# Optimization experiments

Measured on AMD Instinct MI355X. Metric: run time of the kernel, lower is better.

Reference implementation:

```python
import jax, jax.numpy as jnp
import numpy as np

B, G, N_IN, N_HID, N_OUT = 2, 4096, 8, 32, 32
ALPHA, BETA, BN_EPS = 0.005, 5e-5, 1e-5
EDGE_P = 0.05  # adjacency density


def _lin_init(k, fan_in, fan_out):
    k1, k2 = jax.random.split(k)
    lim = 1.0 / np.sqrt(fan_in)
    W = jax.random.uniform(k1, (fan_in, fan_out), minval=-lim, maxval=lim, dtype=jnp.float32)
    b = jax.random.uniform(k2, (fan_out,), minval=-lim, maxval=lim, dtype=jnp.float32)
    return W, b


def setup_inputs() -> dict:
    key = jax.random.key(0)
    ks = jax.random.split(key, 12)
    W_infer, b_infer = _lin_init(ks[0], N_IN, N_HID)
    W_e1, b_e1 = _lin_init(ks[1], 2 * N_HID, 1)
    W_e2, b_e2 = _lin_init(ks[2], 2 * N_HID, 1)
    W_n1, b_n1 = _lin_init(ks[3], 2 * N_HID, N_OUT)
    W_n2, b_n2 = _lin_init(ks[4], 2 * N_HID, N_OUT)
    W_m1, b_m1 = _lin_init(ks[5], 2 * N_HID, N_OUT)
    W_m2, b_m2 = _lin_init(ks[6], 2 * N_HID, N_OUT)
    x = jax.random.normal(ks[7], (B, G, N_IN), dtype=jnp.float32)
    edges1 = jax.random.bernoulli(ks[8], EDGE_P, (G, G)).astype(jnp.float32)
    edges2 = jax.random.bernoulli(ks[9], EDGE_P, (G, G)).astype(jnp.float32)
    bn_gamma = jnp.ones((G,), jnp.float32)
    bn_beta = jnp.zeros((G,), jnp.float32)
    return dict(x=x, edges1=edges1, edges2=edges2, W_infer=W_infer, b_infer=b_infer,
                W_e1=W_e1, b_e1=b_e1, W_e2=W_e2, b_e2=b_e2,
                W_n1=W_n1, b_n1=b_n1, W_n2=W_n2, b_n2=b_n2,
                W_m1=W_m1, b_m1=b_m1, W_m2=W_m2, b_m2=b_m2,
                bn_gamma=bn_gamma, bn_beta=bn_beta)


def _mp_block(x, adj, coef, W_e, b_e, W_n, b_n, W_m, b_m):
    # x: [B,G,H]. Torch builds edge feature at flat index k=i*G+j as cat([x_j, x_i])
    # (shape2 = col gather, shape1 = row gather). We keep the same math without
    # materializing the [B,G*G,2H] tensor.
    Hh = x.shape[-1]
    s_src = x @ W_e[:Hh]   # [B,G,1]  (x_j part of mlp_edge)
    s_dst = x @ W_e[Hh:]   # [B,G,1]  (x_i part of mlp_edge)
    logits = s_dst[:, :, None, 0] + s_src[:, None, :, 0] + b_e[0]   # [B,G,G] at (i,j)
    w = adj + coef * (adj == 0).astype(x.dtype)                     # ori_edge + coef*thres_edge
    e = jax.nn.sigmoid(logits) * w[None]                            # [B,G,G]
    # receive at node i: sum_j e_ij * [x_j, x_i]
    recv_src = jnp.einsum('bij,bjh->bih', e, x)                     # sum_j e_ij x_j
    recv_dst = x * jnp.sum(e, axis=2)[..., None]                    # x_i * sum_j e_ij
    recv = jnp.concatenate([recv_src, recv_dst], axis=-1)           # [B,G,2H]
    recv = jax.nn.elu(recv @ W_n + b_n)                             # nodes_mlp + elu
    upd = jnp.concatenate([recv, x], axis=-1) @ W_m + b_m           # mesg_merge (mode='cat')
    return jax.nn.elu(upd)


def _forward(x, edges1, edges2, W_infer, b_infer, W_e1, b_e1, W_e2, b_e2,
             W_n1, b_n1, W_n2, b_n2, W_m1, b_m1, W_m2, b_m2, bn_gamma, bn_beta):
    h = jax.nn.elu(x @ W_infer + b_infer)                           # infer + elu, [B,G,H]
    h = _mp_block(h, edges1, ALPHA, W_e1, b_e1, W_n1, b_n1, W_m1, b_m1)
    # BatchNorm1d(gene_num) on [B, G, n_out]: per-gene stats over (batch, feature)
    mu = jnp.mean(h, axis=(0, 2), keepdims=True)
    var = jnp.var(h, axis=(0, 2), keepdims=True)
    h = (h - mu) * jax.lax.rsqrt(var + BN_EPS)
    h = h * bn_gamma[None, :, None] + bn_beta[None, :, None]
    return _mp_block(h, edges2, BETA, W_e2, b_e2, W_n2, b_n2, W_m2, b_m2)


def reference(x, edges1, edges2, W_infer, b_infer, W_e1, b_e1, W_e2, b_e2,
              W_n1, b_n1, W_n2, b_n2, W_m1, b_m1, W_m2, b_m2, bn_gamma, bn_beta):
    return _forward(x, edges1, edges2, W_infer, b_infer, W_e1, b_e1, W_e2, b_e2,
                    W_n1, b_n1, W_n2, b_n2, W_m1, b_m1, W_m2, b_m2, bn_gamma, bn_beta)
```

## Files before the change

kernel.cpp:

```cpp
#include <hip/hip_runtime.h>

#define G 4096
#define BSZ 2
#define NIN 8
#define HID 32
#define NLOG2E (-1.4426950408889634f)

typedef __attribute__((ext_vector_type(8))) short short8;
typedef __attribute__((ext_vector_type(4))) float floatx4;
typedef unsigned short ushort_t;
typedef unsigned int uint_t;

__device__ __forceinline__ float elu1(float v) {
    return v > 0.f ? v : (__expf(v) - 1.f);
}
__device__ __forceinline__ ushort_t f2bf(float f) {
    unsigned u = __float_as_uint(f);
    u += 0x7fffu + ((u >> 16) & 1u);
    return (ushort_t)(u >> 16);
}

__global__ __launch_bounds__(256) void k_setup1(
    const float* __restrict__ x, const float* __restrict__ W,
    const float* __restrict__ bias, const float* __restrict__ We,
    float* __restrict__ h0, ushort_t* __restrict__ hTb,
    float* __restrict__ ssrc, float* __restrict__ sdst) {
    __shared__ __align__(16) ushort_t hs[HID][264];
    int tid = threadIdx.x;
    int t = blockIdx.x * 256 + tid;
    int b = t >> 12;
    int g0 = (blockIdx.x & 15) * 256;
    float xin[NIN];
    const float* xp = x + t * NIN;
#pragma unroll
    for (int k = 0; k < NIN; k++) xin[k] = xp[k];
    float ss = 0.f, sd = 0.f;
    float* hp = h0 + (size_t)t * HID;
#pragma unroll
    for (int o = 0; o < HID; o++) {
        float v = bias[o];
#pragma unroll
        for (int k = 0; k < NIN; k++) v += xin[k] * W[k * HID + o];
        v = elu1(v);
        hp[o] = v;
        hs[o][tid] = f2bf(v);
        ss += v * We[o];
        sd += v * We[HID + o];
    }
    ssrc[t] = exp2f(ss * NLOG2E);
    sdst[t] = sd * NLOG2E;
    __syncthreads();
#pragma unroll
    for (int p = 0; p < 4; p++) {
        int row = p * 8 + (tid >> 5);
        int c = (tid & 31) * 8;
        short8 v8 = *(const short8*)&hs[row][c];
        *(short8*)(void*)&hTb[(size_t)(b * HID + row) * G + g0 + c] = v8;
    }
}

__global__ __launch_bounds__(512, 2) void k_mp(
    const float* __restrict__ adj, const float* __restrict__ ssrc,
    const float* __restrict__ sdst, const ushort_t* __restrict__ hTb_in,
    const float* __restrict__ bep, float coef, float* __restrict__ pr) {
    __shared__ __align__(16) float ssm[BSZ][1024];
    __shared__ __align__(16) uint_t abits[32][17];
    __shared__ __align__(16) float red[6][64][9];

    int tid = threadIdx.x;
    int gblk = blockIdx.x >> 2, jh = blockIdx.x & 3;
    int g0 = gblk * 16, j0 = jh * 1024;
    int l = tid & 63, w = tid >> 6;
    int b = w >> 2, jq = w & 3;
    int m = l & 15, kg = l >> 4;

    int jstart = j0 + jq * 256;
    const ushort_t* hb0 = hTb_in + (size_t)(b * HID + m) * G + jstart + kg * 8;
    const ushort_t* hb1 = hb0 + (size_t)16 * G;
    short8 pb0[2], pb1[2];
#pragma unroll
    for (int d = 0; d < 2; d++) {
        pb0[d] = *(const short8*)(const void*)(hb0 + d * 32);
        pb1[d] = *(const short8*)(const void*)(hb1 + d * 32);
    }

    {
        int bb = tid >> 8, j4 = tid & 255;
        *(float4*)&ssm[bb][j4 * 4] = *(const float4*)&ssrc[bb * G + j0 + j4 * 4];
    }
    {
        int r = tid >> 8, f4 = tid & 255;
        int word = f4 >> 3;
        int sh2 = (tid & 7) * 4;
        bool st = (tid & 7) == 0;
        float4 ld[4];
#pragma unroll
        for (int half = 0; half < 2; half++) {
#pragma unroll
            for (int q = 0; q < 4; q++)
                ld[q] = *(const float4*)&adj[(size_t)(g0 + (half * 4 + q) * 2 + r) * G +
                                             j0 + f4 * 4];
#pragma unroll
            for (int q = 0; q < 4; q++) {
                float4 v4 = ld[q];
                uint_t nib = (uint_t)(v4.x != 0.f) | ((uint_t)(v4.y != 0.f) << 1) |
                             ((uint_t)(v4.z != 0.f) << 2) | ((uint_t)(v4.w != 0.f) << 3);
                uint_t wd = nib << sh2;
                wd |= __shfl_xor(wd, 1);
                wd |= __shfl_xor(wd, 2);
                wd |= __shfl_xor(wd, 4);
                if (st) abits[word][(half * 4 + q) * 2 + r] = wd;
            }
        }
    }

    float Dv = exp2f(sdst[b * G + g0 + m] + bep[0] * NLOG2E);
    const float wm1 = 1.f - coef;
    floatx4 c0 = {0.f, 0.f, 0.f, 0.f}, c1 = {0.f, 0.f, 0.f, 0.f};
    float es = 0.f;
    __syncthreads();

    const float* svp = &ssm[b][jq * 256 + kg * 8];
    float4 sv0[2], sv1[2];
    uint_t bwr[2];
#pragma unroll
    for (int d = 0; d < 2; d++) {
        sv0[d] = *(const float4*)&svp[d * 32];
        sv1[d] = *(const float4*)&svp[d * 32 + 4];
        bwr[d] = abits[jq * 8 + d][m];
    }

#pragma unroll
    for (int jc = 0; jc < 8; jc++) {
        int lc = jc & 1;
        short8 bf0 = pb0[lc], bf1 = pb1[lc];
        float4 s0 = sv0[lc], s1 = sv1[lc];
        uint_t bw = bwr[lc];
        if (jc + 2 < 8) {
            pb0[lc] = *(const short8*)(const void*)(hb0 + (jc + 2) * 32);
            pb1[lc] = *(const short8*)(const void*)(hb1 + (jc + 2) * 32);
            sv0[lc] = *(const float4*)&svp[(jc + 2) * 32];
            sv1[lc] = *(const float4*)&svp[(jc + 2) * 32 + 4];
            bwr[lc] = abits[jq * 8 + jc + 2][m];
        }
        float ev[8] = {s0.x, s0.y, s0.z, s0.w, s1.x, s1.y, s1.z, s1.w};
        short8 af;
#pragma unroll
        for (int t8 = 0; t8 < 8; t8++) {
            float bitf = (float)((bw >> (kg * 8 + t8)) & 1u);
            float wgt = __builtin_fmaf(bitf, wm1, coef);
            float ex = Dv * ev[t8];
            float e = __builtin_amdgcn_rcpf(1.f + ex) * wgt;
            es += e;
            af[t8] = (short)(__float_as_uint(e) >> 16);
        }
        c0 = __builtin_amdgcn_mfma_f32_16x16x32_bf16(af, bf0, c0, 0, 0, 0);
        c1 = __builtin_amdgcn_mfma_f32_16x16x32_bf16(af, bf1, c1, 0, 0, 0);
    }

    if (jq) {
        int widx = b * 3 + jq - 1;
#pragma unroll
        for (int r = 0; r < 4; r++) {
            red[widx][l][r] = c0[r];
            red[widx][l][4 + r] = c1[r];
        }
        red[widx][l][8] = es;
    }
    __syncthreads();
    if (!jq) {
#pragma unroll
        for (int q = 0; q < 3; q++) {
            int widx = b * 3 + q;
#pragma unroll
            for (int r = 0; r < 4; r++) {
                c0[r] += red[widx][l][r];
                c1[r] += red[widx][l][4 + r];
            }
            es += red[widx][l][8];
        }
        es += __shfl_xor(es, 16);
        es += __shfl_xor(es, 32);
        float* prb = pr + (size_t)blockIdx.x * 1056;
#pragma unroll
        for (int r = 0; r < 4; r++) {
            int gene = (l >> 4) * 4 + r;
            int row = gene * 2 + b;
            prb[row * 32 + m] = c0[r];
            prb[row * 32 + 16 + m] = c1[r];
        }
        if (l < 16) prb[1024 + l * 2 + b] = es;
    }
}

template <bool DO_BN>
__global__ __launch_bounds__(1024, 4) void k_post(
    const float* __restrict__ pr, const float* __restrict__ hin,
    const float* __restrict__ Wn, const float* __restrict__ bnb,
    const float* __restrict__ Wm, const float* __restrict__ bmb,
    const float* __restrict__ gamma, const float* __restrict__ beta,
    const float* __restrict__ We2, float* __restrict__ outp,
    ushort_t* __restrict__ hTb_out, float* __restrict__ s2s,
    float* __restrict__ s2d) {
    __shared__ __align__(16) float rec[32][68];
    __shared__ __align__(16) float rec2[32][68];
    __shared__ __align__(16) ushort_t tb[BSZ][HID][16];
    __shared__ __align__(16) float Wns[2048];
    __shared__ __align__(16) float Wms[2048];

    int tid = threadIdx.x;
    int g0 = blockIdx.x * 16;
    if (tid < 512) {
        ((float4*)Wns)[tid] = ((const float4*)Wn)[tid];
    } else {
        ((float4*)Wms)[tid - 512] = ((const float4*)Wm)[tid - 512];
    }
    int rl = tid >> 5, hh = tid & 31;
    int gene = rl >> 1, bb = rl & 1;
    const float* p0 = pr + (size_t)blockIdx.x * 4 * 1056;
    float rv = p0[rl * 32 + hh] + p0[1056 + rl * 32 + hh] +
               p0[2112 + rl * 32 + hh] + p0[3168 + rl * 32 + hh];
    float esv = p0[1024 + rl] + p0[1056 + 1024 + rl] +
                p0[2112 + 1024 + rl] + p0[3168 + 1024 + rl];
    float xv = hin[((size_t)(bb * G + g0 + gene)) * HID + hh];
    rec[rl][hh] = rv;
    rec[rl][32 + hh] = xv * esv;
    __syncthreads();

    float v = bnb[hh];
#pragma unroll
    for (int k4 = 0; k4 < 16; k4++) {
        float4 r4 = *(const float4*)&rec[rl][k4 * 4];
        v += r4.x * Wns[(k4 * 4 + 0) * HID + hh];
        v += r4.y * Wns[(k4 * 4 + 1) * HID + hh];
        v += r4.z * Wns[(k4 * 4 + 2) * HID + hh];
        v += r4.w * Wns[(k4 * 4 + 3) * HID + hh];
    }
    v = elu1(v);
    rec2[rl][hh] = v;
    rec2[rl][32 + hh] = xv;
    float u = bmb[hh];
#pragma unroll
    for (int k4 = 0; k4 < 16; k4++) {
        float4 r4 = *(const float4*)&rec2[rl][k4 * 4];
        u += r4.x * Wms[(k4 * 4 + 0) * HID + hh];
        u += r4.y * Wms[(k4 * 4 + 1) * HID + hh];
        u += r4.z * Wms[(k4 * 4 + 2) * HID + hh];
        u += r4.w * Wms[(k4 * 4 + 3) * HID + hh];
    }
    float h1v = elu1(u);
    if (!DO_BN) {
        outp[((size_t)(bb * G + g0 + gene)) * HID + hh] = h1v;
    } else {
        float s = h1v, sq = h1v * h1v;
#pragma unroll
        for (int mm = 32; mm; mm >>= 1) {
            s += __shfl_xor(s, mm);
            sq += __shfl_xor(sq, mm);
        }
        float mu = s * (1.f / 64.f);
        float var = sq * (1.f / 64.f) - mu * mu;
        float rstd = rsqrtf(var + 1e-5f);
        float hn = (h1v - mu) * rstd * gamma[g0 + gene] + beta[g0 + gene];
        outp[((size_t)(bb * G + g0 + gene)) * HID + hh] = hn;
        tb[bb][hh][gene] = f2bf(hn);
        float ps = hn * We2[hh], pd = hn * We2[HID + hh];
#pragma unroll
        for (int mm = 16; mm; mm >>= 1) {
            ps += __shfl_xor(ps, mm);
            pd += __shfl_xor(pd, mm);
        }
        if (hh == 0) {
            s2s[bb * G + g0 + gene] = exp2f(ps * NLOG2E);
            s2d[bb * G + g0 + gene] = pd * NLOG2E;
        }
        __syncthreads();
        if (tid < 128) {
            int b2 = tid >> 6, c = (tid >> 1) & 31, half = tid & 1;
            short8 v8 = *(const short8*)&tb[b2][c][half * 8];
            *(short8*)(void*)&hTb_out[(size_t)(b2 * HID + c) * G + g0 + half * 8] = v8;
        }
    }
}

extern "C" void kernel_launch(void* const* d_in, const int* in_sizes, int n_in,
                              void* d_out, int out_size, void* d_ws, size_t ws_size,
                              hipStream_t stream) {
    const float* x      = (const float*)d_in[0];
    const float* edges1 = (const float*)d_in[1];
    const float* edges2 = (const float*)d_in[2];
    const float* W_inf  = (const float*)d_in[3];
    const float* b_inf  = (const float*)d_in[4];
    const float* W_e1   = (const float*)d_in[5];
    const float* b_e1   = (const float*)d_in[6];
    const float* W_e2   = (const float*)d_in[7];
    const float* b_e2   = (const float*)d_in[8];
    const float* W_n1   = (const float*)d_in[9];
    const float* b_n1   = (const float*)d_in[10];
    const float* W_n2   = (const float*)d_in[11];
    const float* b_n2   = (const float*)d_in[12];
    const float* W_m1   = (const float*)d_in[13];
    const float* b_m1   = (const float*)d_in[14];
    const float* W_m2   = (const float*)d_in[15];
    const float* b_m2   = (const float*)d_in[16];
    const float* bn_g   = (const float*)d_in[17];
    const float* bn_b   = (const float*)d_in[18];
    float* out = (float*)d_out;

    float* ws = (float*)d_ws;
    float* h0   = ws;
    float* h1n  = ws + 262144;
    float* s1s  = ws + 524288;
    float* s1d  = ws + 532480;
    float* s2s  = ws + 540672;
    float* s2d  = ws + 548864;
    ushort_t* hTb  = (ushort_t*)(ws + 557056);
    ushort_t* hTb2 = (ushort_t*)(ws + 688128);
    float* pr = ws + 819200;

    const float ALPHA = 0.005f, BETA = 5e-5f;

    k_setup1<<<32, 256, 0, stream>>>(x, W_inf, b_inf, W_e1, h0, hTb, s1s, s1d);
    k_mp<<<1024, 512, 0, stream>>>(edges1, s1s, s1d, hTb, b_e1, ALPHA, pr);
    k_post<true><<<256, 1024, 0, stream>>>(
        pr, h0, W_n1, b_n1, W_m1, b_m1, bn_g, bn_b, W_e2,
        h1n, hTb2, s2s, s2d);
    k_mp<<<1024, 512, 0, stream>>>(edges2, s2s, s2d, hTb2, b_e2, BETA, pr);
    k_post<false><<<256, 1024, 0, stream>>>(
        pr, h1n, W_n2, b_n2, W_m2, b_m2, nullptr, nullptr, nullptr,
        out, nullptr, nullptr, nullptr);
}
```

Measured before the change: 219.2 us.

## Pack second adjacency into bitmask inside first message-passing kernel

The first message-passing kernel additionally streams the second layer's float adjacency, software-pipelined across its MFMA loop, and writes it as a packed bitmask to workspace. The second message-passing kernel then loads only the packed bits instead of reading and converting the full float adjacency. This moves the large edges2 read into a kernel where it can overlap with compute, at the cost of extra loads, shuffles and register pressure in the first kernel.

Result: slower. 231.1 us (+5.4%).

```diff
diff --git a/kernel.cpp b/kernel.cpp
--- a/kernel.cpp
+++ b/kernel.cpp
@@ -59,10 +59,13 @@
     }
 }
 
+template <int MODE>
 __global__ __launch_bounds__(512, 2) void k_mp(
-    const float* __restrict__ adj, const float* __restrict__ ssrc,
-    const float* __restrict__ sdst, const ushort_t* __restrict__ hTb_in,
-    const float* __restrict__ bep, float coef, float* __restrict__ pr) {
+    const float* __restrict__ adj, const uint_t* __restrict__ pkin,
+    const float* __restrict__ e2src, uint_t* __restrict__ pkout,
+    const float* __restrict__ ssrc, const float* __restrict__ sdst,
+    const ushort_t* __restrict__ hTb_in, const float* __restrict__ bep,
+    float coef, float* __restrict__ pr) {
     __shared__ __align__(16) float ssm[BSZ][1024];
     __shared__ __align__(16) uint_t abits[32][17];
     __shared__ __align__(16) float red[6][64][9];
@@ -74,6 +77,11 @@
     int b = w >> 2, jq = w & 3;
     int m = l & 15, kg = l >> 4;
 
+    const int e2r = tid >> 8, e2c = tid & 255;
+    float4 e2n;
+    if (MODE == 1)
+        e2n = *(const float4*)&e2src[(size_t)(g0 + e2r) * G + j0 + e2c * 4];
+
     int jstart = j0 + jq * 256;
     const ushort_t* hb0 = hTb_in + (size_t)(b * HID + m) * G + jstart + kg * 8;
     const ushort_t* hb1 = hb0 + (size_t)16 * G;
@@ -88,7 +96,7 @@
         int bb = tid >> 8, j4 = tid & 255;
         *(float4*)&ssm[bb][j4 * 4] = *(const float4*)&ssrc[bb * G + j0 + j4 * 4];
     }
-    {
+    if (MODE == 1) {
         int r = tid >> 8, f4 = tid & 255;
         int word = f4 >> 3;
         int sh2 = (tid & 7) * 4;
@@ -112,6 +120,9 @@
                 if (st) abits[word][(half * 4 + q) * 2 + r] = wd;
             }
         }
+    } else {
+        int row = tid >> 5, wq = tid & 31;
+        abits[wq][row] = pkin[(size_t)(g0 + row) * 128 + jh * 32 + wq];
     }
 
     float Dv = exp2f(sdst[b * G + g0 + m] + bep[0] * NLOG2E);
@@ -136,6 +147,13 @@
         short8 bf0 = pb0[lc], bf1 = pb1[lc];
         float4 s0 = sv0[lc], s1 = sv1[lc];
         uint_t bw = bwr[lc];
+        float4 e2cur;
+        if (MODE == 1) {
+            e2cur = e2n;
+            if (jc + 1 < 8)
+                e2n = *(const float4*)&e2src[(size_t)(g0 + 2 * (jc + 1) + e2r) * G +
+                                             j0 + e2c * 4];
+        }
         if (jc + 2 < 8) {
             pb0[lc] = *(const short8*)(const void*)(hb0 + (jc + 2) * 32);
             pb1[lc] = *(const short8*)(const void*)(hb1 + (jc + 2) * 32);
@@ -156,6 +174,16 @@
         }
         c0 = __builtin_amdgcn_mfma_f32_16x16x32_bf16(af, bf0, c0, 0, 0, 0);
         c1 = __builtin_amdgcn_mfma_f32_16x16x32_bf16(af, bf1, c1, 0, 0, 0);
+        if (MODE == 1) {
+            uint_t nib = (uint_t)(e2cur.x != 0.f) | ((uint_t)(e2cur.y != 0.f) << 1) |
+                         ((uint_t)(e2cur.z != 0.f) << 2) | ((uint_t)(e2cur.w != 0.f) << 3);
+            uint_t wd = nib << ((tid & 7) * 4);
+            wd |= __shfl_xor(wd, 1);
+            wd |= __shfl_xor(wd, 2);
+            wd |= __shfl_xor(wd, 4);
+            if ((tid & 7) == 0)
+                pkout[(size_t)(g0 + 2 * jc + e2r) * 128 + jh * 32 + (e2c >> 3)] = wd;
+        }
     }
 
     if (jq) {
@@ -317,15 +345,18 @@
     ushort_t* hTb  = (ushort_t*)(ws + 557056);
     ushort_t* hTb2 = (ushort_t*)(ws + 688128);
     float* pr = ws + 819200;
+    uint_t* pk2 = (uint_t*)(ws + 1900544);
 
     const float ALPHA = 0.005f, BETA = 5e-5f;
 
     k_setup1<<<32, 256, 0, stream>>>(x, W_inf, b_inf, W_e1, h0, hTb, s1s, s1d);
-    k_mp<<<1024, 512, 0, stream>>>(edges1, s1s, s1d, hTb, b_e1, ALPHA, pr);
+    k_mp<1><<<1024, 512, 0, stream>>>(
+        edges1, nullptr, edges2, pk2, s1s, s1d, hTb, b_e1, ALPHA, pr);
     k_post<true><<<256, 1024, 0, stream>>>(
         pr, h0, W_n1, b_n1, W_m1, b_m1, bn_g, bn_b, W_e2,
         h1n, hTb2, s2s, s2d);
-    k_mp<<<1024, 512, 0, stream>>>(edges2, s2s, s2d, hTb2, b_e2, BETA, pr);
+    k_mp<0><<<1024, 512, 0, stream>>>(
+        nullptr, pk2, nullptr, nullptr, s2s, s2d, hTb2, b_e2, BETA, pr);
     k_post<false><<<256, 1024, 0, stream>>>(
         pr, h1n, W_n2, b_n2, W_m2, b_m2, nullptr, nullptr, nullptr,
         out, nullptr, nullptr, nullptr);
```
